# Kernel tuning notes

Hardware: AMD Instinct MI355X
Metric: run time of the kernel (lower is better)

The kernel has to match this reference:

```python
import jax, jax.numpy as jnp
import numpy as np

N = 100000      # nodes
E = 3200000     # edges (avg degree 32)
NFEAT, NHID, NCLASS, PROJ = 512, 256, 64, 128


def setup_inputs() -> dict:
    key = jax.random.key(0)
    ks = jax.random.split(key, 8)
    x = jax.random.normal(ks[0], (N, NFEAT), dtype=jnp.float32)
    rows = jax.random.randint(ks[1], (E,), 0, N)
    cols = jax.random.randint(ks[2], (E,), 0, N)
    # symmetric-normalized adjacency weights are O(1/deg); uniform/32 mimics that scale
    vals = jax.random.uniform(ks[3], (E,), dtype=jnp.float32) * (1.0 / 32.0)
    W1 = jax.random.normal(ks[4], (NFEAT, NHID), dtype=jnp.float32) / np.sqrt(NFEAT).astype(np.float32)
    b1 = jnp.zeros((NHID,), jnp.float32)
    W2 = jax.random.normal(ks[5], (NHID, NCLASS), dtype=jnp.float32) / np.sqrt(NHID).astype(np.float32)
    b2 = jnp.zeros((NCLASS,), jnp.float32)
    W3 = jax.random.normal(ks[6], (NCLASS, PROJ), dtype=jnp.float32) / np.sqrt(NCLASS).astype(np.float32)
    b3 = jnp.zeros((PROJ,), jnp.float32)
    return {"x": x, "vals": vals, "W1": W1, "b1": b1, "W2": W2, "b2": b2,
            "W3": W3, "b3": b3, "rows": rows, "cols": cols, "encoder_type": 0}


def spmm(rows, cols, vals, h):
    # y[i] = sum_{e: rows[e]==i} vals[e] * h[cols[e]]   (COO spmm == torch.spmm(adj, h))
    return jax.ops.segment_sum(vals[:, None] * h[cols], rows, num_segments=N)


def reference(x, vals, W1, b1, W2, b2, W3, b3, rows, cols, encoder_type):
    # encoder_type == 0 path (eval mode: dropout is identity)
    # gc1: spmm(adj, x @ W1) + b1  -> relu
    h = jax.nn.relu(spmm(rows, cols, vals, x @ W1) + b1)     # [N, NHID]
    # gc2: spmm(adj, h @ W2) + b2
    z = spmm(rows, cols, vals, h @ W2) + b2                  # [N, NCLASS]
    # fc3(relu(z))
    out = jax.nn.relu(z) @ W3 + b3                           # [N, PROJ]
    return jax.nn.log_softmax(z, axis=1), out
```

## Files before the change

### kernel.cpp

```cpp
#include <hip/hip_runtime.h>

static constexpr int NN = 100000;
static constexpr int NE = 3200000;
static constexpr int KF = 512;
static constexpr int NH = 256;
static constexpr int NC = 64;
static constexpr int NP = 128;

typedef __attribute__((ext_vector_type(4))) float f32x4;
typedef __attribute__((ext_vector_type(8))) __bf16 bf16x8;

__device__ __forceinline__ unsigned short f2bf(float f) {
  unsigned u = __builtin_bit_cast(unsigned, f);
  u += 0x7fffu + ((u >> 16) & 1u);
  return (unsigned short)(u >> 16);
}
__device__ __forceinline__ float bf2f(unsigned short h) {
  return __builtin_bit_cast(float, (unsigned)h << 16);
}

__global__ void hist_k(const int* __restrict__ rows, int* __restrict__ cnt) {
  int stride = gridDim.x * blockDim.x;
  for (int e = blockIdx.x * blockDim.x + threadIdx.x; e < NE; e += stride)
    atomicAdd(&cnt[rows[e]], 1);
}

__global__ __launch_bounds__(256) void scanA_k(const int* __restrict__ cnt,
                                               int* __restrict__ partial,
                                               int* __restrict__ bsums) {
  __shared__ int ts[256];
  const int t = threadIdx.x;
  const int base = blockIdx.x * 1024 + t * 4;
  int v[4]; int s = 0;
#pragma unroll
  for (int j = 0; j < 4; j++) { v[j] = (base + j < NN) ? cnt[base + j] : 0; s += v[j]; }
  ts[t] = s; __syncthreads();
  for (int off = 1; off < 256; off <<= 1) {
    int x2 = (t >= off) ? ts[t - off] : 0;
    __syncthreads();
    ts[t] += x2;
    __syncthreads();
  }
  int excl = ts[t] - s;
#pragma unroll
  for (int j = 0; j < 4; j++) {
    if (base + j < NN) partial[base + j] = excl;
    excl += v[j];
  }
  if (t == 255) bsums[blockIdx.x] = ts[255];
}

__global__ __launch_bounds__(128) void scanB_k(const int* __restrict__ bsums,
                                               int* __restrict__ offs, int nb) {
  __shared__ int ts[128];
  const int t = threadIdx.x;
  int v = (t < nb) ? bsums[t] : 0;
  ts[t] = v; __syncthreads();
  for (int off = 1; off < 128; off <<= 1) {
    int x2 = (t >= off) ? ts[t - off] : 0;
    __syncthreads();
    ts[t] += x2;
    __syncthreads();
  }
  if (t < nb) offs[t] = ts[t] - v;
}

__global__ __launch_bounds__(256) void scanC_k(int* __restrict__ row_ptr,
                                               int* __restrict__ cursor,
                                               const int* __restrict__ offs) {
  const int t = threadIdx.x;
  const int base = blockIdx.x * 1024 + t * 4;
  const int off = offs[blockIdx.x];
#pragma unroll
  for (int j = 0; j < 4; j++) {
    if (base + j < NN) {
      int vv = row_ptr[base + j] + off;
      row_ptr[base + j] = vv;
      cursor[base + j] = vv;
    }
  }
  if (blockIdx.x == 0 && t == 0) row_ptr[NN] = NE;
}

__global__ void scatter_k(const int* __restrict__ rows, const int* __restrict__ cols,
                          const float* __restrict__ vals, int* __restrict__ cur,
                          uint2* __restrict__ edge_s) {
  int stride = gridDim.x * blockDim.x;
  for (int e = blockIdx.x * blockDim.x + threadIdx.x; e < NE; e += stride) {
    int pos = atomicAdd(&cur[rows[e]], 1);
    edge_s[pos] = make_uint2((unsigned)cols[e], __builtin_bit_cast(unsigned, vals[e]));
  }
}

__global__ __launch_bounds__(256) void gemm1_mfma(const float* __restrict__ x,
                                                  const float* __restrict__ W1,
                                                  unsigned short* __restrict__ t1b) {
  constexpr int LDA = 72;
  __shared__ unsigned short As[128 * LDA];
  __shared__ unsigned short Bs[128 * LDA];
  const int tid = threadIdx.x;
  const int m0 = blockIdx.x * 128;
  const int n0 = blockIdx.y * 128;
  const int w = tid >> 6, lane = tid & 63;
  const int wm = w & 1, wn = w >> 1;
  const int quad = lane >> 4, l16 = lane & 15;

  f32x4 acc[4][4] = {};

  for (int ks = 0; ks < 8; ks++) {
    __syncthreads();
#pragma unroll
    for (int i = 0; i < 8; i++) {
      int it = tid + 256 * i;
      int row = it >> 4;
      int k4 = (it & 15) * 4;
      int gr = m0 + row; if (gr > NN - 1) gr = NN - 1;
      const float4 v = *(const float4*)(x + (size_t)gr * KF + ks * 64 + k4);
      unsigned lo = (unsigned)f2bf(v.x) | ((unsigned)f2bf(v.y) << 16);
      unsigned hi = (unsigned)f2bf(v.z) | ((unsigned)f2bf(v.w) << 16);
      *(uint2*)&As[row * LDA + k4] = make_uint2(lo, hi);
    }
#pragma unroll
    for (int i = 0; i < 8; i++) {
      int it = tid + 256 * i;
      int n = it & 127;
      int k4 = (it >> 7) * 4;
      int gk = ks * 64 + k4;
      float v0 = W1[(size_t)(gk + 0) * NH + n0 + n];
      float v1 = W1[(size_t)(gk + 1) * NH + n0 + n];
      float v2 = W1[(size_t)(gk + 2) * NH + n0 + n];
      float v3 = W1[(size_t)(gk + 3) * NH + n0 + n];
      unsigned lo = (unsigned)f2bf(v0) | ((unsigned)f2bf(v1) << 16);
      unsigned hi = (unsigned)f2bf(v2) | ((unsigned)f2bf(v3) << 16);
      *(uint2*)&Bs[n * LDA + k4] = make_uint2(lo, hi);
    }
    __syncthreads();
#pragma unroll
    for (int kk = 0; kk < 2; kk++) {
      bf16x8 a[4], b[4];
#pragma unroll
      for (int mt = 0; mt < 4; mt++) {
        const uint4 q = *(const uint4*)&As[(wm * 64 + mt * 16 + l16) * LDA + kk * 32 + quad * 8];
        a[mt] = __builtin_bit_cast(bf16x8, q);
      }
#pragma unroll
      for (int nt = 0; nt < 4; nt++) {
        const uint4 q = *(const uint4*)&Bs[(wn * 64 + nt * 16 + l16) * LDA + kk * 32 + quad * 8];
        b[nt] = __builtin_bit_cast(bf16x8, q);
      }
#pragma unroll
      for (int mt = 0; mt < 4; mt++)
#pragma unroll
        for (int nt = 0; nt < 4; nt++)
          acc[mt][nt] = __builtin_amdgcn_mfma_f32_16x16x32_bf16(a[mt], b[nt], acc[mt][nt], 0, 0, 0);
    }
  }
#pragma unroll
  for (int mt = 0; mt < 4; mt++) {
#pragma unroll
    for (int reg = 0; reg < 4; reg++) {
      int row = m0 + wm * 64 + mt * 16 + quad * 4 + reg;
      if (row < NN) {
#pragma unroll
        for (int nt = 0; nt < 4; nt++) {
          int col = n0 + wn * 64 + nt * 16 + l16;
          t1b[(size_t)row * NH + col] = f2bf(acc[mt][nt][reg]);
        }
      }
    }
  }
}

__global__ __launch_bounds__(256) void spmm1_relu(const unsigned short* __restrict__ t1b,
                                                  const uint2* __restrict__ edge,
                                                  const int* __restrict__ row_ptr,
                                                  const float* __restrict__ b1,
                                                  unsigned short* __restrict__ hb) {
  const int w = threadIdx.x >> 6, lane = threadIdx.x & 63;
  const int r = blockIdx.x * 4 + w;
  int s = row_ptr[r], e = row_ptr[r + 1];
  s = __builtin_amdgcn_readfirstlane(s);
  e = __builtin_amdgcn_readfirstlane(e);
  float a0 = 0.f, a1 = 0.f, a2 = 0.f, a3 = 0.f;
  for (int i = s; i < e; i += 8) {
    uint2 ed[8];
#pragma unroll
    for (int j = 0; j < 8; j++) {
      const int idx = i + j;
      uint2 t = edge[idx < e ? idx : (e - 1)];
      if (idx >= e) t.y = 0u;
      ed[j] = t;
    }
    uint2 d[8];
#pragma unroll
    for (int j = 0; j < 8; j++)
      d[j] = *(const uint2*)(t1b + (size_t)ed[j].x * NH + lane * 4);
#pragma unroll
    for (int j = 0; j < 8; j++) {
      const float v = __builtin_bit_cast(float, ed[j].y);
      a0 += v * bf2f((unsigned short)(d[j].x & 0xffffu));
      a1 += v * bf2f((unsigned short)(d[j].x >> 16));
      a2 += v * bf2f((unsigned short)(d[j].y & 0xffffu));
      a3 += v * bf2f((unsigned short)(d[j].y >> 16));
    }
  }
  const int col = lane * 4;
  a0 = fmaxf(a0 + b1[col + 0], 0.f);
  a1 = fmaxf(a1 + b1[col + 1], 0.f);
  a2 = fmaxf(a2 + b1[col + 2], 0.f);
  a3 = fmaxf(a3 + b1[col + 3], 0.f);
  unsigned lo = (unsigned)f2bf(a0) | ((unsigned)f2bf(a1) << 16);
  unsigned hi = (unsigned)f2bf(a2) | ((unsigned)f2bf(a3) << 16);
  *(uint2*)(hb + (size_t)r * NH + col) = make_uint2(lo, hi);
}

__global__ __launch_bounds__(256) void gemm2_mfma(const unsigned short* __restrict__ hb,
                                                  const float* __restrict__ W2,
                                                  unsigned short* __restrict__ t2b) {
  constexpr int LDB = 264;
  __shared__ unsigned short Bs[64 * LDB];
  const int tid = threadIdx.x;
#pragma unroll
  for (int i = 0; i < 16; i++) {
    int it = tid + 256 * i;
    int n = it & 63;
    int k4 = (it >> 6) * 4;
    float v0 = W2[(size_t)(k4 + 0) * NC + n];
    float v1 = W2[(size_t)(k4 + 1) * NC + n];
    float v2 = W2[(size_t)(k4 + 2) * NC + n];
    float v3 = W2[(size_t)(k4 + 3) * NC + n];
    unsigned lo = (unsigned)f2bf(v0) | ((unsigned)f2bf(v1) << 16);
    unsigned hi = (unsigned)f2bf(v2) | ((unsigned)f2bf(v3) << 16);
    *(uint2*)&Bs[n * LDB + k4] = make_uint2(lo, hi);
  }
  __syncthreads();
  const int w = tid >> 6, lane = tid & 63;
  const int quad = lane >> 4, l16 = lane & 15;
  const int m0 = blockIdx.x * 256 + w * 64;
  f32x4 acc[4][4] = {};
  const unsigned short* ap[4];
#pragma unroll
  for (int mt = 0; mt < 4; mt++) {
    int r = m0 + mt * 16 + l16; if (r > NN - 1) r = NN - 1;
    ap[mt] = hb + (size_t)r * NH + quad * 8;
  }
  for (int ks = 0; ks < 8; ks++) {
    bf16x8 a[4], b[4];
#pragma unroll
    for (int mt = 0; mt < 4; mt++) {
      const uint4 q = *(const uint4*)(ap[mt] + ks * 32);
      a[mt] = __builtin_bit_cast(bf16x8, q);
    }
#pragma unroll
    for (int nt = 0; nt < 4; nt++) {
      const uint4 q = *(const uint4*)&Bs[(nt * 16 + l16) * LDB + ks * 32 + quad * 8];
      b[nt] = __builtin_bit_cast(bf16x8, q);
    }
#pragma unroll
    for (int mt = 0; mt < 4; mt++)
#pragma unroll
      for (int nt = 0; nt < 4; nt++)
        acc[mt][nt] = __builtin_amdgcn_mfma_f32_16x16x32_bf16(a[mt], b[nt], acc[mt][nt], 0, 0, 0);
  }
#pragma unroll
  for (int mt = 0; mt < 4; mt++) {
#pragma unroll
    for (int reg = 0; reg < 4; reg++) {
      int row = m0 + mt * 16 + quad * 4 + reg;
      if (row < NN) {
#pragma unroll
        for (int nt = 0; nt < 4; nt++) {
          int col = nt * 16 + l16;
          t2b[(size_t)row * NC + col] = f2bf(acc[mt][nt][reg]);
        }
      }
    }
  }
}

__global__ __launch_bounds__(256) void spmm2_fused(const unsigned short* __restrict__ t2b,
                                                   const uint2* __restrict__ edge,
                                                   const int* __restrict__ row_ptr,
                                                   const float* __restrict__ b2,
                                                   const float* __restrict__ W3,
                                                   const float* __restrict__ b3,
                                                   float* __restrict__ out0,
                                                   float* __restrict__ out1) {
  __shared__ float W3s[NC * NP];
  __shared__ float rz[4][NC];
  for (int it = threadIdx.x; it < NC * NP / 4; it += 256)
    ((float4*)W3s)[it] = ((const float4*)W3)[it];
  const int w = threadIdx.x >> 6, lane = threadIdx.x & 63;
  const int r = blockIdx.x * 4 + w;
  int s = row_ptr[r], e = row_ptr[r + 1];
  s = __builtin_amdgcn_readfirstlane(s);
  e = __builtin_amdgcn_readfirstlane(e);
  float acc = 0.f;
  for (int i = s; i < e; i += 8) {
    uint2 ed[8];
#pragma unroll
    for (int j = 0; j < 8; j++) {
      const int idx = i + j;
      uint2 t = edge[idx < e ? idx : (e - 1)];
      if (idx >= e) t.y = 0u;
      ed[j] = t;
    }
    float g[8];
#pragma unroll
    for (int j = 0; j < 8; j++)
      g[j] = bf2f(t2b[(size_t)ed[j].x * NC + lane]);
#pragma unroll
    for (int j = 0; j < 8; j++)
      acc += __builtin_bit_cast(float, ed[j].y) * g[j];
  }
  const float z = acc + b2[lane];
  float m = z;
#pragma unroll
  for (int off = 32; off > 0; off >>= 1) m = fmaxf(m, __shfl_xor(m, off, 64));
  const float ex = expf(z - m);
  float sum = ex;
#pragma unroll
  for (int off = 32; off > 0; off >>= 1) sum += __shfl_xor(sum, off, 64);
  out0[(size_t)r * NC + lane] = z - m - logf(sum);
  rz[w][lane] = fmaxf(z, 0.f);
  __syncthreads();
  float o0 = b3[lane], o1 = b3[64 + lane];
#pragma unroll 8
  for (int k = 0; k < NC; k++) {
    const float rk = rz[w][k];
    o0 += rk * W3s[k * NP + lane];
    o1 += rk * W3s[k * NP + 64 + lane];
  }
  out1[(size_t)r * NP + lane] = o0;
  out1[(size_t)r * NP + 64 + lane] = o1;
}

extern "C" void kernel_launch(void* const* d_in, const int* in_sizes, int n_in,
                              void* d_out, int out_size, void* d_ws, size_t ws_size,
                              hipStream_t stream) {
  const float* x    = (const float*)d_in[0];
  const float* vals = (const float*)d_in[1];
  const float* W1   = (const float*)d_in[2];
  const float* b1   = (const float*)d_in[3];
  const float* W2   = (const float*)d_in[4];
  const float* b2   = (const float*)d_in[5];
  const float* W3   = (const float*)d_in[6];
  const float* b3   = (const float*)d_in[7];
  const int* rows   = (const int*)d_in[8];
  const int* cols   = (const int*)d_in[9];

  char* ws = (char*)d_ws;
  unsigned short* t1b = (unsigned short*)(ws + 0);
  unsigned short* hb  = (unsigned short*)(ws + 51200000);
  unsigned short* t2b = (unsigned short*)(ws + 102400000);
  uint2* edge_s       = (uint2*)(ws + 115200000);
  int*   row_ptr      = (int*)(ws + 140800000);
  int*   cursor       = (int*)(ws + 141201152);
  int*   bsums        = (int*)(ws + 141601280);
  int*   offs         = (int*)(ws + 141601792);

  float* out0 = (float*)d_out;
  float* out1 = out0 + (size_t)NN * NC;

  const int SCAN_BLKS = (NN + 1023) / 1024;

  hipMemsetAsync(cursor, 0, (size_t)NN * sizeof(int), stream);
  hist_k<<<2048, 256, 0, stream>>>(rows, cursor);
  scanA_k<<<SCAN_BLKS, 256, 0, stream>>>(cursor, row_ptr, bsums);
  scanB_k<<<1, 128, 0, stream>>>(bsums, offs, SCAN_BLKS);
  scanC_k<<<SCAN_BLKS, 256, 0, stream>>>(row_ptr, cursor, offs);
  scatter_k<<<2048, 256, 0, stream>>>(rows, cols, vals, cursor, edge_s);

  gemm1_mfma<<<dim3((NN + 127) / 128, 2), 256, 0, stream>>>(x, W1, t1b);
  spmm1_relu<<<NN / 4, 256, 0, stream>>>(t1b, edge_s, row_ptr, b1, hb);
  gemm2_mfma<<<(NN + 255) / 256, 256, 0, stream>>>(hb, W2, t2b);
  spmm2_fused<<<NN / 4, 256, 0, stream>>>(t2b, edge_s, row_ptr, b2, W3, b3, out0, out1);
}
```

Before: 1.282 ms.

## Replace global-atomic COO-to-CSR scatter with two-phase bucketed binning

Builds CSR in two passes. The first pass bins edges into buckets of 128 rows, using per-block shared-memory histograms and one global atomic per bucket per tile. The second pass does a per-bucket row histogram and a localized scatter, so global atomics and writes stay inside a small row range. This is meant to cut the contention and cache misses of random per-edge global atomics in the old hist and scatter kernels. The cost is an extra pass over a staging buffer that aliases t1b space, plus more kernel launches.

```diff
diff --git a/kernel.cpp b/kernel.cpp
--- a/kernel.cpp
+++ b/kernel.cpp
@@ -7,6 +7,10 @@
 static constexpr int NC = 64;
 static constexpr int NP = 128;
 
+static constexpr int NB = 782;
+static constexpr int TILE = 16384;
+static constexpr int NTILES = (NE + TILE - 1) / TILE;
+
 typedef __attribute__((ext_vector_type(4))) float f32x4;
 typedef __attribute__((ext_vector_type(8))) __bf16 bf16x8;
 
@@ -19,10 +23,94 @@
   return __builtin_bit_cast(float, (unsigned)h << 16);
 }
 
-__global__ void hist_k(const int* __restrict__ rows, int* __restrict__ cnt) {
-  int stride = gridDim.x * blockDim.x;
-  for (int e = blockIdx.x * blockDim.x + threadIdx.x; e < NE; e += stride)
-    atomicAdd(&cnt[rows[e]], 1);
+__global__ __launch_bounds__(256) void bhist_k(const int* __restrict__ rows,
+                                               int* __restrict__ bcnt) {
+  __shared__ int cnt[NB];
+  for (int i = threadIdx.x; i < NB; i += 256) cnt[i] = 0;
+  __syncthreads();
+  const int e0 = blockIdx.x * TILE;
+  for (int i = threadIdx.x; i < TILE; i += 256) {
+    int e = e0 + i;
+    if (e < NE) atomicAdd(&cnt[rows[e] >> 7], 1);
+  }
+  __syncthreads();
+  for (int i = threadIdx.x; i < NB; i += 256)
+    if (cnt[i] > 0) atomicAdd(&bcnt[i], cnt[i]);
+}
+
+__global__ __launch_bounds__(256) void bscan_k(const int* __restrict__ bcnt,
+                                               int* __restrict__ bucket_ptr,
+                                               int* __restrict__ bcur) {
+  __shared__ int ts[256];
+  const int t = threadIdx.x;
+  const int base = t * 4;
+  int v[4]; int ssum = 0;
+#pragma unroll
+  for (int j = 0; j < 4; j++) { v[j] = (base + j < NB) ? bcnt[base + j] : 0; ssum += v[j]; }
+  ts[t] = ssum; __syncthreads();
+  for (int off = 1; off < 256; off <<= 1) {
+    int x2 = (t >= off) ? ts[t - off] : 0;
+    __syncthreads();
+    ts[t] += x2;
+    __syncthreads();
+  }
+  int excl = ts[t] - ssum;
+#pragma unroll
+  for (int j = 0; j < 4; j++) {
+    if (base + j < NB) { bucket_ptr[base + j] = excl; bcur[base + j] = excl; }
+    excl += v[j];
+  }
+  if (t == 255) bucket_ptr[NB] = NE;
+}
+
+__global__ __launch_bounds__(256) void phase1_bin(const int* __restrict__ rows,
+                                                  const int* __restrict__ cols,
+                                                  const float* __restrict__ vals,
+                                                  int* __restrict__ bcur,
+                                                  uint2* __restrict__ stage) {
+  __shared__ int cnt[NB];
+  __shared__ int gpos[NB];
+  const int t = threadIdx.x;
+  const int e0 = blockIdx.x * TILE;
+  for (int i = t; i < NB; i += 256) cnt[i] = 0;
+  __syncthreads();
+  for (int i = t; i < TILE; i += 256) {
+    int e = e0 + i;
+    if (e < NE) atomicAdd(&cnt[rows[e] >> 7], 1);
+  }
+  __syncthreads();
+  for (int b = t; b < NB; b += 256) {
+    int c = cnt[b];
+    gpos[b] = (c > 0) ? atomicAdd(&bcur[b], c) : 0;
+    cnt[b] = 0;
+  }
+  __syncthreads();
+  for (int i = t; i < TILE; i += 256) {
+    int e = e0 + i;
+    if (e < NE) {
+      int r = rows[e];
+      int b = r >> 7;
+      int rank = atomicAdd(&cnt[b], 1);
+      unsigned w0 = ((unsigned)(r & 127) << 17) | (unsigned)cols[e];
+      stage[gpos[b] + rank] = make_uint2(w0, __builtin_bit_cast(unsigned, vals[e]));
+    }
+  }
+}
+
+__global__ __launch_bounds__(256) void rowhist_k(const uint2* __restrict__ stage,
+                                                 const int* __restrict__ bucket_ptr,
+                                                 int* __restrict__ row_cnt) {
+  __shared__ int cnt[128];
+  const int b = blockIdx.x;
+  const int t = threadIdx.x;
+  if (t < 128) cnt[t] = 0;
+  __syncthreads();
+  const int s = bucket_ptr[b], e = bucket_ptr[b + 1];
+  for (int i = s + t; i < e; i += 256)
+    atomicAdd(&cnt[stage[i].x >> 17], 1);
+  __syncthreads();
+  int row = b * 128 + t;
+  if (t < 128 && row < NN) row_cnt[row] = cnt[t];
 }
 
 __global__ __launch_bounds__(256) void scanA_k(const int* __restrict__ cnt,
@@ -82,13 +170,24 @@
   if (blockIdx.x == 0 && t == 0) row_ptr[NN] = NE;
 }
 
-__global__ void scatter_k(const int* __restrict__ rows, const int* __restrict__ cols,
-                          const float* __restrict__ vals, int* __restrict__ cur,
-                          uint2* __restrict__ edge_s) {
-  int stride = gridDim.x * blockDim.x;
-  for (int e = blockIdx.x * blockDim.x + threadIdx.x; e < NE; e += stride) {
-    int pos = atomicAdd(&cur[rows[e]], 1);
-    edge_s[pos] = make_uint2((unsigned)cols[e], __builtin_bit_cast(unsigned, vals[e]));
+__global__ __launch_bounds__(256) void phase2_k(const uint2* __restrict__ stage,
+                                                const int* __restrict__ bucket_ptr,
+                                                int* __restrict__ cursor,
+                                                uint2* __restrict__ edge_s) {
+  const int b = blockIdx.x;
+  const int base = b * 128;
+  const int s = bucket_ptr[b], e = bucket_ptr[b + 1];
+  for (int i0 = s + threadIdx.x * 4; i0 < e; i0 += 1024) {
+#pragma unroll
+    for (int j = 0; j < 4; j++) {
+      int idx = i0 + j;
+      if (idx < e) {
+        uint2 rec = stage[idx];
+        int row = base + (int)(rec.x >> 17);
+        int pos = atomicAdd(&cursor[row], 1);
+        edge_s[pos] = make_uint2(rec.x & 0x1FFFFu, rec.y);
+      }
+    }
   }
 }
 
@@ -351,25 +450,33 @@
 
   char* ws = (char*)d_ws;
   unsigned short* t1b = (unsigned short*)(ws + 0);
+  uint2* stage        = (uint2*)(ws + 0);
   unsigned short* hb  = (unsigned short*)(ws + 51200000);
   unsigned short* t2b = (unsigned short*)(ws + 102400000);
   uint2* edge_s       = (uint2*)(ws + 115200000);
   int*   row_ptr      = (int*)(ws + 140800000);
-  int*   cursor       = (int*)(ws + 141201152);
-  int*   bsums        = (int*)(ws + 141601280);
-  int*   offs         = (int*)(ws + 141601792);
+  int*   cursor       = (int*)(ws + 141200128);
+  int*   row_cnt      = (int*)(ws + 141600128);
+  int*   bsums        = (int*)(ws + 142000128);
+  int*   offs         = (int*)(ws + 142000640);
+  int*   bcnt         = (int*)(ws + 142001152);
+  int*   bucket_ptr   = (int*)(ws + 142004352);
+  int*   bcur         = (int*)(ws + 142007552);
 
   float* out0 = (float*)d_out;
   float* out1 = out0 + (size_t)NN * NC;
 
   const int SCAN_BLKS = (NN + 1023) / 1024;
 
-  hipMemsetAsync(cursor, 0, (size_t)NN * sizeof(int), stream);
-  hist_k<<<2048, 256, 0, stream>>>(rows, cursor);
-  scanA_k<<<SCAN_BLKS, 256, 0, stream>>>(cursor, row_ptr, bsums);
+  hipMemsetAsync(bcnt, 0, NB * sizeof(int), stream);
+  bhist_k<<<NTILES, 256, 0, stream>>>(rows, bcnt);
+  bscan_k<<<1, 256, 0, stream>>>(bcnt, bucket_ptr, bcur);
+  phase1_bin<<<NTILES, 256, 0, stream>>>(rows, cols, vals, bcur, stage);
+  rowhist_k<<<NB, 256, 0, stream>>>(stage, bucket_ptr, row_cnt);
+  scanA_k<<<SCAN_BLKS, 256, 0, stream>>>(row_cnt, row_ptr, bsums);
   scanB_k<<<1, 128, 0, stream>>>(bsums, offs, SCAN_BLKS);
   scanC_k<<<SCAN_BLKS, 256, 0, stream>>>(row_ptr, cursor, offs);
-  scatter_k<<<2048, 256, 0, stream>>>(rows, cols, vals, cursor, edge_s);
+  phase2_k<<<NB, 256, 0, stream>>>(stage, bucket_ptr, cursor, edge_s);
 
   gemm1_mfma<<<dim3((NN + 127) / 128, 2), 256, 0, stream>>>(x, W1, t1b);
   spmm1_relu<<<NN / 4, 256, 0, stream>>>(t1b, edge_s, row_ptr, b1, hb);
```

After: 1.129 ms. -12.0%, faster.
